# Kernel optimization log

Hardware: AMD Instinct MI355X
Metric: run time of the kernel (lower is better)

Reference implementation:

```python
import jax, jax.numpy as jnp
import numpy as np


def _sage_layer(x_src, x_dst, src, dst, n_dst, W_neigh, W_self, b):
    # mean aggregation of src features onto dst nodes (zero for isolated dst)
    msgs = x_src[src]                                            # [E, d_in]
    summed = jax.ops.segment_sum(msgs, dst, num_segments=n_dst)  # [n_dst, d_in]
    deg = jax.ops.segment_sum(jnp.ones_like(dst, dtype=x_src.dtype), dst,
                              num_segments=n_dst)                # [n_dst]
    mean = summed / jnp.maximum(deg, 1)[:, None]
    # DGL SAGEConv('mean'): fc_self(h_dst) + fc_neigh(h_mean) + bias
    return x_dst @ W_self + mean @ W_neigh + b


def setup_inputs() -> dict:
    key = jax.random.key(0)
    ks = jax.random.split(key, 12)
    N_SRC, D_IN, HID, OUT = 100000, 128, 256, 64
    SIZE1, SIZE2 = 25000, 5000
    E1, E2 = 800000, 160000

    def glorot(k, shape):
        lim = np.sqrt(6.0 / (shape[0] + shape[1])).astype(np.float32)
        return jax.random.uniform(k, shape, jnp.float32, -lim, lim)

    return {
        "x": jax.random.normal(ks[0], (N_SRC, D_IN), jnp.float32),
        "W_self1": glorot(ks[1], (D_IN, HID)),
        "W_neigh1": glorot(ks[2], (D_IN, HID)),
        "b1": jnp.zeros((HID,), jnp.float32),
        "W_self2": glorot(ks[3], (HID, OUT)),
        "W_neigh2": glorot(ks[4], (HID, OUT)),
        "b2": jnp.zeros((OUT,), jnp.float32),
        "edge_src1": jax.random.randint(ks[5], (E1,), 0, N_SRC, jnp.int32),
        "edge_dst1": jax.random.randint(ks[6], (E1,), 0, SIZE1, jnp.int32),
        "edge_src2": jax.random.randint(ks[7], (E2,), 0, SIZE1, jnp.int32),
        "edge_dst2": jax.random.randint(ks[8], (E2,), 0, SIZE2, jnp.int32),
        "size1": SIZE1,
        "size2": SIZE2,
    }


def reference(x, W_self1, W_neigh1, b1, W_self2, W_neigh2, b2,
              edge_src1, edge_dst1, edge_src2, edge_dst2, size1, size2):
    # Layer 1: src = all nodes, dst = first size1 nodes
    h = _sage_layer(x, x[:size1], edge_src1, edge_dst1, size1,
                    W_neigh1, W_self1, b1)
    h = jax.nn.relu(h)  # dropout is identity in eval mode
    # Layer 2: src = layer-1 outputs (size1 nodes), dst = first size2 nodes
    h = _sage_layer(h, h[:size2], edge_src2, edge_dst2, size2,
                    W_neigh2, W_self2, b2)
    return jax.nn.log_softmax(h, axis=-1)
```

## Files before the change

### kernel.cpp

```cpp
#include <hip/hip_runtime.h>


constexpr int D_IN  = 128;
constexpr int HID   = 256;
constexpr int OUT_D = 64;
constexpr int SIZE1 = 25000;
constexpr int SIZE2 = 5000;
constexpr int SLOTS = 80;

using bf16x8 = __attribute__((ext_vector_type(8))) short;
using f32x4  = __attribute__((ext_vector_type(4))) float;

__device__ inline unsigned short f32_to_bf16_rne(float f) {
    unsigned u = __builtin_bit_cast(unsigned, f);
    u = (u + 0x7fffu + ((u >> 16) & 1u)) >> 16;
    return (unsigned short)u;
}
__device__ inline float bf16_lo(unsigned u) {
    return __builtin_bit_cast(float, u << 16);
}
__device__ inline float bf16_hi(unsigned u) {
    return __builtin_bit_cast(float, u & 0xffff0000u);
}
__device__ inline unsigned pack_bf16(float lo, float hi) {
    return (unsigned)f32_to_bf16_rne(lo) | ((unsigned)f32_to_bf16_rne(hi) << 16);
}
__device__ inline void add8(float* a, uint4 v) {
    a[0] += bf16_lo(v.x); a[1] += bf16_hi(v.x);
    a[2] += bf16_lo(v.y); a[3] += bf16_hi(v.y);
    a[4] += bf16_lo(v.z); a[5] += bf16_hi(v.z);
    a[6] += bf16_lo(v.w); a[7] += bf16_hi(v.w);
}

__global__ void megafuse(const int* __restrict__ es1, const int* __restrict__ ed1,
                         int E1, int* __restrict__ cnt1, int* __restrict__ csr1,
                         const int* __restrict__ es2, const int* __restrict__ ed2,
                         int E2, int* __restrict__ cnt2, int* __restrict__ csr2,
                         const float* __restrict__ x, unsigned* __restrict__ xb,
                         long n4,
                         const float* __restrict__ Ws1, const float* __restrict__ Wn1,
                         const float* __restrict__ Ws2, const float* __restrict__ Wn2,
                         unsigned short* __restrict__ Wt1,
                         unsigned short* __restrict__ Wt2,
                         int f1, int f2, int f3) {
    const int b = blockIdx.x;
    const int tid = threadIdx.x;
    if (b < f1) {
        int base = b * 1024 + tid;
#pragma unroll
        for (int j = 0; j < 4; ++j) {
            int e = base + j * 256;
            if (e < E1) {
                int d = ed1[e];
                int pos = atomicAdd(&cnt1[d], 1);
                if (pos < SLOTS) csr1[d * SLOTS + pos] = es1[e];
            }
        }
    } else if (b < f2) {
        int base = (b - f1) * 1024 + tid;
#pragma unroll
        for (int j = 0; j < 4; ++j) {
            int e = base + j * 256;
            if (e < E2) {
                int d = ed2[e];
                int pos = atomicAdd(&cnt2[d], 1);
                if (pos < SLOTS) csr2[d * SLOTS + pos] = es2[e];
            }
        }
    } else if (b < f3) {
        long i0 = (long)(b - f2) * 512 + tid;
#pragma unroll
        for (int j = 0; j < 2; ++j) {
            long i = i0 + j * 256;
            if (i < n4) {
                float4 v = reinterpret_cast<const float4*>(x)[i];
                uint2 o;
                o.x = pack_bf16(v.x, v.y);
                o.y = pack_bf16(v.z, v.w);
                reinterpret_cast<uint2*>(xb)[i] = o;
            }
        }
    } else {
        int i = (b - f3) * 256 + tid;
        if (i < HID * (2 * D_IN)) {
            int n = i >> 8, k = i & 255;
            float v = (k < D_IN) ? Ws1[k * HID + n] : Wn1[(k - D_IN) * HID + n];
            Wt1[i] = f32_to_bf16_rne(v);
        } else {
            int j = i - HID * (2 * D_IN);
            if (j < OUT_D * (2 * HID)) {
                int n = j >> 9, k = j & 511;
                float v = (k < HID) ? Ws2[k * OUT_D + n] : Wn2[(k - HID) * OUT_D + n];
                Wt2[j] = f32_to_bf16_rne(v);
            }
        }
    }
}

template <int QPL>
__global__ void agg_pull2(const uint4* __restrict__ X4,
                          const int* __restrict__ csr,
                          const int* __restrict__ cnt,
                          uint4* __restrict__ mean4, int ndst) {
    constexpr int R4 = QPL * 16;
    const int wid = threadIdx.x >> 6;
    const int lane = threadIdx.x & 63;
    const int d = blockIdx.x * 4 + wid;
    if (d >= ndst) return;
    const int n = min(cnt[d], SLOTS);
    const int beg = d * SLOTS;
    const int end = beg + n;
    const int g = lane >> 4;
    const int c = lane & 15;

    float acc[QPL][8];
#pragma unroll
    for (int q = 0; q < QPL; ++q)
#pragma unroll
        for (int j = 0; j < 8; ++j) acc[q][j] = 0.0f;

    int e = beg + g;
    for (; e + 12 < end; e += 16) {
        int s0 = csr[e], s1 = csr[e + 4], s2 = csr[e + 8], s3 = csr[e + 12];
#pragma unroll
        for (int q = 0; q < QPL; ++q) {
            uint4 v0 = X4[(long)s0 * R4 + q * 16 + c];
            uint4 v1 = X4[(long)s1 * R4 + q * 16 + c];
            uint4 v2 = X4[(long)s2 * R4 + q * 16 + c];
            uint4 v3 = X4[(long)s3 * R4 + q * 16 + c];
            add8(acc[q], v0); add8(acc[q], v1); add8(acc[q], v2); add8(acc[q], v3);
        }
    }
    for (; e < end; e += 4) {
        long s0 = csr[e];
#pragma unroll
        for (int q = 0; q < QPL; ++q) {
            uint4 v0 = X4[s0 * R4 + q * 16 + c];
            add8(acc[q], v0);
        }
    }
#pragma unroll
    for (int q = 0; q < QPL; ++q)
#pragma unroll
        for (int j = 0; j < 8; ++j) {
            acc[q][j] += __shfl_xor(acc[q][j], 16);
            acc[q][j] += __shfl_xor(acc[q][j], 32);
        }
    if (g == 0) {
        const float inv = 1.0f / (float)max(n, 1);
#pragma unroll
        for (int q = 0; q < QPL; ++q) {
            uint4 o;
            o.x = pack_bf16(acc[q][0] * inv, acc[q][1] * inv);
            o.y = pack_bf16(acc[q][2] * inv, acc[q][3] * inv);
            o.z = pack_bf16(acc[q][4] * inv, acc[q][5] * inv);
            o.w = pack_bf16(acc[q][6] * inv, acc[q][7] * inv);
            mean4[(long)d * R4 + q * 16 + c] = o;
        }
    }
}

template <int KPH, bool RELU, bool OUT_BF16, bool LSM>
__global__ __launch_bounds__(256) void sage_gemm_mfma(
    const unsigned short* __restrict__ Aself,
    const unsigned short* __restrict__ Amean,
    const unsigned short* __restrict__ Wt,
    const float* __restrict__ bias,
    void* __restrict__ Cout, int M, int N) {
    constexpr int BM = 64, BN = 64;
    constexpr int ITERS = (BM * KPH) / (256 * 8);
    __shared__ unsigned short As[BM * KPH];
    __shared__ unsigned short Bs[BN * KPH];

    const int tid = threadIdx.x;
    const int wid = tid >> 6;
    const int lane = tid & 63;
    const int wm = wid >> 1, wn = wid & 1;
    const int rowBase = blockIdx.x * BM;
    const int colBase = blockIdx.y * BN;

    f32x4 acc[2][2];
#pragma unroll
    for (int a = 0; a < 2; ++a)
#pragma unroll
        for (int b = 0; b < 2; ++b)
#pragma unroll
            for (int j = 0; j < 4; ++j) acc[a][b][j] = 0.0f;

#pragma unroll
    for (int p = 0; p < 2; ++p) {
        const unsigned short* __restrict__ A = p ? Amean : Aself;
        __syncthreads();
#pragma unroll
        for (int it = 0; it < ITERS; ++it) {
            int flat = (it * 256 + tid) * 8;
            int r = flat / KPH, kc = flat % KPH;
            int gr = rowBase + r;
            if (gr >= M) gr = M - 1;
            uint4 v = *reinterpret_cast<const uint4*>(&A[(long)gr * KPH + kc]);
            int idx = (r * KPH + kc) ^ ((r & 7) << 3);
            *reinterpret_cast<uint4*>(&As[idx]) = v;
        }
#pragma unroll
        for (int it = 0; it < ITERS; ++it) {
            int flat = (it * 256 + tid) * 8;
            int r = flat / KPH, kc = flat % KPH;
            uint4 v = *reinterpret_cast<const uint4*>(
                &Wt[(long)(colBase + r) * (2 * KPH) + p * KPH + kc]);
            int idx = (r * KPH + kc) ^ ((r & 7) << 3);
            *reinterpret_cast<uint4*>(&Bs[idx]) = v;
        }
        __syncthreads();
#pragma unroll
        for (int kk = 0; kk < KPH / 32; ++kk) {
            bf16x8 a[2], b[2];
            const int kb = kk * 32 + 8 * (lane >> 4);
#pragma unroll
            for (int f = 0; f < 2; ++f) {
                int r = wm * 32 + f * 16 + (lane & 15);
                int ia = (r * KPH + kb) ^ ((r & 7) << 3);
                a[f] = *reinterpret_cast<const bf16x8*>(&As[ia]);
                int rn = wn * 32 + f * 16 + (lane & 15);
                int ib = (rn * KPH + kb) ^ ((rn & 7) << 3);
                b[f] = *reinterpret_cast<const bf16x8*>(&Bs[ib]);
            }
#pragma unroll
            for (int fm = 0; fm < 2; ++fm)
#pragma unroll
                for (int fn = 0; fn < 2; ++fn)
                    acc[fm][fn] = __builtin_amdgcn_mfma_f32_16x16x32_bf16(
                        a[fm], b[fn], acc[fm][fn], 0, 0, 0);
        }
    }

    if (LSM) {
        float* sm = reinterpret_cast<float*>(As);
        __syncthreads();
#pragma unroll
        for (int fm = 0; fm < 2; ++fm)
#pragma unroll
            for (int fn = 0; fn < 2; ++fn) {
                int c = wn * 32 + fn * 16 + (lane & 15);
                float bv = bias[colBase + c];
#pragma unroll
                for (int j = 0; j < 4; ++j) {
                    int r = wm * 32 + fm * 16 + 4 * (lane >> 4) + j;
                    sm[r * BN + c] = acc[fm][fn][j] + bv;
                }
            }
        __syncthreads();
        for (int rr = 0; rr < 16; ++rr) {
            int r = wid * 16 + rr;
            int gr = rowBase + r;
            if (gr >= M) continue;
            float v = sm[r * BN + lane];
            float m = v;
#pragma unroll
            for (int o = 32; o; o >>= 1) m = fmaxf(m, __shfl_xor(m, o));
            float ex = __expf(v - m);
            float s = ex;
#pragma unroll
            for (int o = 32; o; o >>= 1) s += __shfl_xor(s, o);
            ((float*)Cout)[(long)gr * N + lane] = v - m - __logf(s);
        }
    } else {
#pragma unroll
        for (int fm = 0; fm < 2; ++fm) {
#pragma unroll
            for (int fn = 0; fn < 2; ++fn) {
                int gc = colBase + wn * 32 + fn * 16 + (lane & 15);
                float bv = bias[gc];
#pragma unroll
                for (int j = 0; j < 4; ++j) {
                    int gr = rowBase + wm * 32 + fm * 16 + 4 * (lane >> 4) + j;
                    if (gr < M) {
                        float v = acc[fm][fn][j] + bv;
                        if (RELU) v = fmaxf(v, 0.0f);
                        if (OUT_BF16)
                            ((unsigned short*)Cout)[(long)gr * N + gc] =
                                f32_to_bf16_rne(v);
                        else
                            ((float*)Cout)[(long)gr * N + gc] = v;
                    }
                }
            }
        }
    }
}


extern "C" void kernel_launch(void* const* d_in, const int* in_sizes, int n_in,
                              void* d_out, int out_size, void* d_ws, size_t ws_size,
                              hipStream_t stream) {
    const float* x       = (const float*)d_in[0];
    const float* Wself1  = (const float*)d_in[1];
    const float* Wneigh1 = (const float*)d_in[2];
    const float* b1      = (const float*)d_in[3];
    const float* Wself2  = (const float*)d_in[4];
    const float* Wneigh2 = (const float*)d_in[5];
    const float* b2      = (const float*)d_in[6];
    const int* es1 = (const int*)d_in[7];
    const int* ed1 = (const int*)d_in[8];
    const int* es2 = (const int*)d_in[9];
    const int* ed2 = (const int*)d_in[10];
    const int E1 = in_sizes[7];
    const int E2 = in_sizes[9];
    const long NSRC = in_sizes[0] / D_IN;

    int* cnt1 = (int*)d_ws;
    int* cnt2 = cnt1 + SIZE1;
    int* csr1 = cnt2 + SIZE2;
    int* csr2 = csr1 + (size_t)SIZE1 * SLOTS;
    size_t int_elems = (size_t)SIZE1 + SIZE2 +
                       (size_t)SIZE1 * SLOTS + (size_t)SIZE2 * SLOTS;
    int_elems = (int_elems + 3) & ~(size_t)3;
    unsigned short* xb    = (unsigned short*)((int*)d_ws + int_elems);
    unsigned short* mean2 = xb;
    unsigned short* Wt1   = xb + NSRC * D_IN;
    unsigned short* Wt2   = Wt1 + (size_t)HID * (2 * D_IN);
    unsigned short* mean1 = Wt2 + (size_t)OUT_D * (2 * HID);
    unsigned short* h1    = mean1 + (size_t)SIZE1 * D_IN;

    hipMemsetAsync(d_ws, 0, (SIZE1 + SIZE2) * sizeof(int), stream);

    const long n4 = NSRC * D_IN / 4;
    const int f1 = (E1 + 1023) / 1024;
    const int f2 = f1 + (E2 + 1023) / 1024;
    const int f3 = f2 + (int)((n4 + 511) / 512);
    const int nb_cw = (HID * (2 * D_IN) + OUT_D * (2 * HID) + 255) / 256;
    megafuse<<<f3 + nb_cw, 256, 0, stream>>>(
        es1, ed1, E1, cnt1, csr1, es2, ed2, E2, cnt2, csr2,
        x, (unsigned*)xb, n4, Wself1, Wneigh1, Wself2, Wneigh2, Wt1, Wt2,
        f1, f2, f3);

    agg_pull2<1><<<(SIZE1 + 3) / 4, 256, 0, stream>>>(
        (const uint4*)xb, csr1, cnt1, (uint4*)mean1, SIZE1);
    {
        dim3 grid((SIZE1 + 63) / 64, HID / 64);
        sage_gemm_mfma<D_IN, true, true, false><<<grid, 256, 0, stream>>>(
            xb, mean1, Wt1, b1, h1, SIZE1, HID);
    }

    agg_pull2<2><<<(SIZE2 + 3) / 4, 256, 0, stream>>>(
        (const uint4*)h1, csr2, cnt2, (uint4*)mean2, SIZE2);
    {
        dim3 grid((SIZE2 + 63) / 64, OUT_D / 64);
        sage_gemm_mfma<HID, false, false, true><<<grid, 256, 0, stream>>>(
            h1, mean2, Wt2, b2, d_out, SIZE2, OUT_D);
    }
}
```

Measured before the change: 152.4 us.

## Partition CSR build atomics by XCD slice and unroll gather loop deeper

Result: no change. 154.5 us (+1.3%).

```diff
diff --git a/kernel.cpp b/kernel.cpp
--- a/kernel.cpp
+++ b/kernel.cpp
@@ -7,6 +7,10 @@
 constexpr int SIZE1 = 25000;
 constexpr int SIZE2 = 5000;
 constexpr int SLOTS = 80;
+constexpr int NXCD  = 8;
+constexpr int SLICE1 = (SIZE1 + NXCD - 1) / NXCD;
+constexpr int SLICE2 = (SIZE2 + NXCD - 1) / NXCD;
+constexpr int ECH = 2048;
 
 using bf16x8 = __attribute__((ext_vector_type(8))) short;
 using f32x4  = __attribute__((ext_vector_type(4))) float;
@@ -46,25 +50,32 @@
     const int b = blockIdx.x;
     const int tid = threadIdx.x;
     if (b < f1) {
-        int base = b * 1024 + tid;
-#pragma unroll
-        for (int j = 0; j < 4; ++j) {
+        const int xcd = b & (NXCD - 1);
+        const int base = (b >> 3) * ECH + tid;
+#pragma unroll
+        for (int j = 0; j < ECH / 256; ++j) {
             int e = base + j * 256;
             if (e < E1) {
                 int d = ed1[e];
-                int pos = atomicAdd(&cnt1[d], 1);
-                if (pos < SLOTS) csr1[d * SLOTS + pos] = es1[e];
+                if (d / SLICE1 == xcd) {
+                    int pos = atomicAdd(&cnt1[d], 1);
+                    if (pos < SLOTS) csr1[d * SLOTS + pos] = es1[e];
+                }
             }
         }
     } else if (b < f2) {
-        int base = (b - f1) * 1024 + tid;
-#pragma unroll
-        for (int j = 0; j < 4; ++j) {
+        const int bb = b - f1;
+        const int xcd = bb & (NXCD - 1);
+        const int base = (bb >> 3) * ECH + tid;
+#pragma unroll
+        for (int j = 0; j < ECH / 256; ++j) {
             int e = base + j * 256;
             if (e < E2) {
                 int d = ed2[e];
-                int pos = atomicAdd(&cnt2[d], 1);
-                if (pos < SLOTS) csr2[d * SLOTS + pos] = es2[e];
+                if (d / SLICE2 == xcd) {
+                    int pos = atomicAdd(&cnt2[d], 1);
+                    if (pos < SLOTS) csr2[d * SLOTS + pos] = es2[e];
+                }
             }
         }
     } else if (b < f3) {
@@ -120,18 +131,29 @@
         for (int j = 0; j < 8; ++j) acc[q][j] = 0.0f;
 
     int e = beg + g;
-    for (; e + 12 < end; e += 16) {
-        int s0 = csr[e], s1 = csr[e + 4], s2 = csr[e + 8], s3 = csr[e + 12];
+    for (; e + 28 < end; e += 32) {
+        int s[8];
+#pragma unroll
+        for (int t = 0; t < 8; ++t) s[t] = csr[e + 4 * t];
+#pragma unroll
+        for (int q = 0; q < QPL; ++q) {
+            uint4 v[8];
+#pragma unroll
+            for (int t = 0; t < 8; ++t) v[t] = X4[(long)s[t] * R4 + q * 16 + c];
+#pragma unroll
+            for (int t = 0; t < 8; ++t) add8(acc[q], v[t]);
+        }
+    }
+    for (; e + 4 < end; e += 8) {
+        int s0 = csr[e], s1 = csr[e + 4];
 #pragma unroll
         for (int q = 0; q < QPL; ++q) {
             uint4 v0 = X4[(long)s0 * R4 + q * 16 + c];
             uint4 v1 = X4[(long)s1 * R4 + q * 16 + c];
-            uint4 v2 = X4[(long)s2 * R4 + q * 16 + c];
-            uint4 v3 = X4[(long)s3 * R4 + q * 16 + c];
-            add8(acc[q], v0); add8(acc[q], v1); add8(acc[q], v2); add8(acc[q], v3);
-        }
-    }
-    for (; e < end; e += 4) {
+            add8(acc[q], v0); add8(acc[q], v1);
+        }
+    }
+    if (e < end) {
         long s0 = csr[e];
 #pragma unroll
         for (int q = 0; q < QPL; ++q) {
@@ -324,8 +346,8 @@
     hipMemsetAsync(d_ws, 0, (SIZE1 + SIZE2) * sizeof(int), stream);
 
     const long n4 = NSRC * D_IN / 4;
-    const int f1 = (E1 + 1023) / 1024;
-    const int f2 = f1 + (E2 + 1023) / 1024;
+    const int f1 = ((E1 + ECH - 1) / ECH) * NXCD;
+    const int f2 = f1 + ((E2 + ECH - 1) / ECH) * NXCD;
     const int f3 = f2 + (int)((n4 + 511) / 512);
     const int nb_cw = (HID * (2 * D_IN) + OUT_D * (2 * HID) + 255) / 256;
     megafuse<<<f3 + nb_cw, 256, 0, stream>>>(
```
